# Optimization experiments

Hardware: AMD Instinct MI355X
Metric: run time of the kernel (lower is better)

Reference implementation:

```python
import jax, jax.numpy as jnp
import numpy as np

INPUT_DIM = 2
COUNT_BINS = 16
BOUND = 5.0
FLOW_LENGTH = 4
HIDDEN = 256
MULT = 4 * COUNT_BINS - 1  # 63 param groups per dim (w:K, h:K, d:K-1, lam:K)
MIN_BIN = 1e-3
MIN_DERIV = 1e-3
MIN_LAMBDA = 0.025
N = 131072


def _masks():
    input_idx = np.arange(1, INPUT_DIM + 1)                  # [2]
    hidden_idx = np.arange(HIDDEN) % (INPUT_DIM - 1) + 1     # all ones for input_dim=2
    out_idx = np.tile(input_idx, MULT)                       # [126] -> [1,2,1,2,...]
    m1 = (hidden_idx[:, None] >= input_idx[None, :]).astype(np.float32)   # [H,2]
    m2 = (hidden_idx[:, None] >= hidden_idx[None, :]).astype(np.float32)  # [H,H]
    m3 = (out_idx[:, None] > hidden_idx[None, :]).astype(np.float32)      # [126,H]
    return jnp.asarray(m1), jnp.asarray(m2), jnp.asarray(m3)


def _made(z, W1, b1, W2, b2, W3, b3, m1, m2, m3):
    # masked MLP producing raw spline params, shape [..., MULT, input_dim]
    h = jax.nn.relu(z @ (W1 * m1).T + b1)
    h = jax.nn.relu(h @ (W2 * m2).T + b2)
    out = (h @ (W3 * m3).T + b3).reshape(z.shape[:-1] + (MULT, INPUT_DIM))
    K = COUNT_BINS
    sw = lambda t: jnp.swapaxes(t, -1, -2)  # -> [..., input_dim, K]
    w = sw(out[..., 0:K, :])
    hh = sw(out[..., K:2 * K, :])
    d = sw(out[..., 2 * K:3 * K - 1, :])
    lam = sw(out[..., 3 * K - 1:4 * K - 1, :])
    return w, hh, d, lam


def _spline(x, w_raw, h_raw, d_raw, l_raw):
    # Pyro monotonic linear rational spline (Dolatabadi et al.), forward only.
    K = COUNT_BINS
    left, right = -BOUND, BOUND
    w = jax.nn.softmax(w_raw, axis=-1)
    h = jax.nn.softmax(h_raw, axis=-1)
    d = jax.nn.softplus(d_raw)
    l = jax.nn.sigmoid(l_raw)

    widths = MIN_BIN + (1.0 - MIN_BIN * K) * w
    zpad = jnp.zeros(widths.shape[:-1] + (1,), widths.dtype)
    cw = jnp.concatenate([zpad, jnp.cumsum(widths, -1)], -1)
    cw = (right - left) * cw + left
    cw = cw.at[..., 0].set(left).at[..., -1].set(right)
    widths = cw[..., 1:] - cw[..., :-1]

    heights = MIN_BIN + (1.0 - MIN_BIN * K) * h
    ch = jnp.concatenate([zpad, jnp.cumsum(heights, -1)], -1)
    ch = (right - left) * ch + left
    ch = ch.at[..., 0].set(left).at[..., -1].set(right)
    heights = ch[..., 1:] - ch[..., :-1]

    deriv = MIN_DERIV + d
    onep = jnp.ones(deriv.shape[:-1] + (1,), deriv.dtype)
    deriv = jnp.concatenate([onep, deriv, onep], -1)  # boundary derivs = 1, [.., K+1]

    lam = MIN_LAMBDA + (1.0 - 2.0 * MIN_LAMBDA) * l

    inside = (x >= left) & (x <= right)
    xc = jnp.clip(x, left, right)

    bin_idx = jnp.clip(jnp.sum((xc[..., None] >= cw).astype(jnp.int32), -1) - 1, 0, K - 1)
    ib = bin_idx[..., None]
    g = lambda t: jnp.take_along_axis(t, ib, -1)[..., 0]
    x_k = g(cw)
    w_k = g(widths)
    y_k = g(ch)
    h_k = g(heights)
    d_k = g(deriv)
    d_k1 = jnp.take_along_axis(deriv, ib + 1, -1)[..., 0]
    lam_k = g(lam)

    wa = 1.0
    wb = jnp.sqrt(d_k / d_k1) * wa
    wc = (lam_k * wa * d_k + (1.0 - lam_k) * wb * d_k1) * (w_k / h_k)
    ya = y_k
    yb = h_k + y_k
    yc = ((1.0 - lam_k) * wa * ya + lam_k * wb * yb) / ((1.0 - lam_k) * wa + lam_k * wb)

    theta = (xc - x_k) / w_k
    left_seg = theta <= lam_k
    num = jnp.where(left_seg,
                    wa * ya * (lam_k - theta) + wc * yc * theta,
                    wc * yc * (1.0 - theta) + wb * yb * (theta - lam_k))
    den = jnp.where(left_seg,
                    wa * (lam_k - theta) + wc * theta,
                    wc * (1.0 - theta) + wb * (theta - lam_k))
    y = num / den
    return jnp.where(inside, y, x)  # identity outside [-B, B]


def setup_inputs() -> dict:
    key = jax.random.key(0)
    ks = jax.random.split(key, 7)
    s = 0.05
    return {
        "x": jax.random.normal(ks[0], (N, INPUT_DIM), jnp.float32),
        "W1": jax.random.normal(ks[1], (HIDDEN, INPUT_DIM), jnp.float32) * s,
        "b1": jax.random.normal(ks[2], (HIDDEN,), jnp.float32) * s,
        "W2": jax.random.normal(ks[3], (HIDDEN, HIDDEN), jnp.float32) * s,
        "b2": jax.random.normal(ks[4], (HIDDEN,), jnp.float32) * s,
        "W3": jax.random.normal(ks[5], (MULT * INPUT_DIM, HIDDEN), jnp.float32) * s,
        "b3": jax.random.normal(ks[6], (MULT * INPUT_DIM,), jnp.float32) * s,
    }


def reference(x, W1, b1, W2, b2, W3, b3):
    # forward(): apply the SAME shared spline transform flow_length times,
    # collecting intermediates zs (returned stacked: [L+1, N, 2]).
    m1, m2, m3 = _masks()
    z = x
    zs = [z]
    for _ in range(FLOW_LENGTH):
        w, hh, d, l = _made(z, W1, b1, W2, b2, W3, b3, m1, m2, m3)
        z = _spline(z, w, hh, d, l)
        zs.append(z)
    return jnp.stack(zs)
```

## Files before the change

kernel.cpp:

```cpp
#include <hip/hip_runtime.h>
#include <math.h>

#define N_SAMPLES 131072
#define HIDDEN    256
#define M_GRID    2048
#define REC       160
#define U_LO      (-8.0f)
#define DELTA     0.0078125f
#define INV_DELTA 128.0f
#define MT3       16

__device__ float g_H2T[M_GRID * HIDDEN];
__device__ float g_table[M_GRID * REC];
__device__ float g_knots0[REC];

__device__ __forceinline__ float rcpf(float x) { return __builtin_amdgcn_rcpf(x); }

__device__ __forceinline__ float softplusf(float x) {
  return fmaxf(x, 0.0f) + log1pf(expf(-fabsf(x)));
}

__device__ void process_column(const float* __restrict__ raw, int stride,
                               float* __restrict__ rec) {
  float v[16];
  float cw[17], ch[17], dv[17], lm[16];
  float mx = -1e30f;
#pragma unroll
  for (int k = 0; k < 16; k++) { v[k] = raw[k * stride]; mx = fmaxf(mx, v[k]); }
  float s = 0.0f;
#pragma unroll
  for (int k = 0; k < 16; k++) { v[k] = expf(v[k] - mx); s += v[k]; }
  float scl = 0.984f / s;
  cw[0] = -5.0f;
  float a = 0.0f;
#pragma unroll
  for (int k = 0; k < 16; k++) {
    a += fmaf(v[k], scl, 0.001f);
    cw[k + 1] = fmaf(a, 10.0f, -5.0f);
  }
  cw[16] = 5.0f;
  mx = -1e30f;
#pragma unroll
  for (int k = 0; k < 16; k++) { v[k] = raw[(16 + k) * stride]; mx = fmaxf(mx, v[k]); }
  s = 0.0f;
#pragma unroll
  for (int k = 0; k < 16; k++) { v[k] = expf(v[k] - mx); s += v[k]; }
  scl = 0.984f / s;
  ch[0] = -5.0f;
  a = 0.0f;
#pragma unroll
  for (int k = 0; k < 16; k++) {
    a += fmaf(v[k], scl, 0.001f);
    ch[k + 1] = fmaf(a, 10.0f, -5.0f);
  }
  ch[16] = 5.0f;
  dv[0] = 1.0f; dv[16] = 1.0f;
#pragma unroll
  for (int j = 0; j < 15; j++) dv[j + 1] = 0.001f + softplusf(raw[(32 + j) * stride]);
#pragma unroll
  for (int k = 0; k < 16; k++) {
    float xx = raw[(47 + k) * stride];
    lm[k] = fmaf(0.95f, 1.0f / (1.0f + expf(-xx)), 0.025f);
  }
  float4* r4 = (float4*)rec;
  r4[0] = make_float4(cw[0], cw[1], cw[2], cw[3]);
  r4[1] = make_float4(cw[4], cw[5], cw[6], cw[7]);
  r4[2] = make_float4(cw[8], cw[9], cw[10], cw[11]);
  r4[3] = make_float4(cw[12], cw[13], cw[14], cw[15]);
  r4[4] = make_float4(cw[16], 0.0f, 0.0f, 0.0f);
#pragma unroll
  for (int k = 0; k < 16; k++) {
    r4[5 + 2 * k] = make_float4(ch[k], ch[k + 1], dv[k], dv[k + 1]);
    r4[6 + 2 * k] = make_float4(lm[k], 0.0f, 0.0f, 0.0f);
  }
}

__device__ __forceinline__ float spline_eval(float z, float xk, float xk1,
                                             float yk, float yk1,
                                             float dk, float dk1, float lam) {
  float xc = fminf(fmaxf(z, -5.0f), 5.0f);
  float wk = xk1 - xk;
  float hk = yk1 - yk;
  float wb = __builtin_amdgcn_sqrtf(dk * rcpf(dk1));
  float wc = fmaf(lam, dk, (1.0f - lam) * wb * dk1) * wk * rcpf(hk);
  float ya = yk;
  float yb = yk + hk;
  float yc = fmaf(lam * wb, yb, (1.0f - lam) * ya) * rcpf(fmaf(lam, wb, 1.0f - lam));
  float th = (xc - xk) * rcpf(wk);
  bool left = th <= lam;
  float num = left ? fmaf(ya, lam - th, wc * yc * th)
                   : fmaf(wc * yc, 1.0f - th, wb * yb * (th - lam));
  float den = left ? fmaf(wc, th, lam - th)
                   : fmaf(wc, 1.0f - th, wb * (th - lam));
  float y = num * rcpf(den);
  bool inside = (z >= -5.0f) && (z <= 5.0f);
  return inside ? y : z;
}

__global__ __launch_bounds__(256) void k_gemm2(const float* __restrict__ W1,
                                               const float* __restrict__ b1,
                                               const float* __restrict__ W2,
                                               const float* __restrict__ b2) {
  __shared__ float sW[256 * 67];
  __shared__ float sH[256 * 36];
  const int t = threadIdx.x;
  const int m0 = blockIdx.x * 32;
  const int o0 = blockIdx.y * 64;
  {
    const int ol = t >> 2, seg = t & 3;
    const float* src = W2 + (size_t)(o0 + ol) * 256 + 16 * seg;
#pragma unroll
    for (int c = 0; c < 4; c++) {
#pragma unroll
      for (int q = 0; q < 4; q++) {
        float4 v = *(const float4*)(src + 64 * c + 4 * q);
        const int k = 64 * c + 16 * seg + 4 * q;
        sW[(k + 0) * 67 + ol] = v.x;
        sW[(k + 1) * 67 + ol] = v.y;
        sW[(k + 2) * 67 + ol] = v.z;
        sW[(k + 3) * 67 + ol] = v.w;
      }
    }
  }
  {
    const float w1v = W1[2 * t];
    const float b1v = b1[t];
#pragma unroll
    for (int q = 0; q < 8; q++) {
      float4 h;
      float u0 = fmaf((float)(m0 + 4 * q + 0), DELTA, U_LO);
      float u1 = fmaf((float)(m0 + 4 * q + 1), DELTA, U_LO);
      float u2 = fmaf((float)(m0 + 4 * q + 2), DELTA, U_LO);
      float u3 = fmaf((float)(m0 + 4 * q + 3), DELTA, U_LO);
      h.x = fmaxf(fmaf(u0, w1v, b1v), 0.0f);
      h.y = fmaxf(fmaf(u1, w1v, b1v), 0.0f);
      h.z = fmaxf(fmaf(u2, w1v, b1v), 0.0f);
      h.w = fmaxf(fmaf(u3, w1v, b1v), 0.0f);
      *(float4*)&sH[t * 36 + 4 * q] = h;
    }
  }
  __syncthreads();
  const int w = t >> 6, lane = t & 63;
  const int tp = lane >> 2, tm = lane & 3;
  float acc[4][8] = {};
  const int kb = w * 64;
#pragma unroll 8
  for (int kk = 0; kk < 64; kk++) {
    const int k = kb + kk;
    float4 av = *(const float4*)&sW[k * 67 + 4 * tp];
    float4 b0 = *(const float4*)&sH[k * 36 + 8 * tm];
    float4 b1v = *(const float4*)&sH[k * 36 + 8 * tm + 4];
#pragma unroll
    for (int i = 0; i < 4; i++) {
      const float a = (i == 0) ? av.x : (i == 1) ? av.y : (i == 2) ? av.z : av.w;
      acc[i][0] = fmaf(a, b0.x, acc[i][0]);
      acc[i][1] = fmaf(a, b0.y, acc[i][1]);
      acc[i][2] = fmaf(a, b0.z, acc[i][2]);
      acc[i][3] = fmaf(a, b0.w, acc[i][3]);
      acc[i][4] = fmaf(a, b1v.x, acc[i][4]);
      acc[i][5] = fmaf(a, b1v.y, acc[i][5]);
      acc[i][6] = fmaf(a, b1v.z, acc[i][6]);
      acc[i][7] = fmaf(a, b1v.w, acc[i][7]);
    }
  }
  __syncthreads();
  if (w > 0) {
#pragma unroll
    for (int i = 0; i < 4; i++) {
      *(float4*)&sH[((w - 1) * 64 + lane) * 36 + 8 * i] =
          make_float4(acc[i][0], acc[i][1], acc[i][2], acc[i][3]);
      *(float4*)&sH[((w - 1) * 64 + lane) * 36 + 8 * i + 4] =
          make_float4(acc[i][4], acc[i][5], acc[i][6], acc[i][7]);
    }
  }
  __syncthreads();
  if (w == 0) {
#pragma unroll
    for (int v = 0; v < 3; v++) {
#pragma unroll
      for (int i = 0; i < 4; i++) {
        float4 r0 = *(const float4*)&sH[(v * 64 + lane) * 36 + 8 * i];
        float4 r1 = *(const float4*)&sH[(v * 64 + lane) * 36 + 8 * i + 4];
        acc[i][0] += r0.x; acc[i][1] += r0.y; acc[i][2] += r0.z; acc[i][3] += r0.w;
        acc[i][4] += r1.x; acc[i][5] += r1.y; acc[i][6] += r1.z; acc[i][7] += r1.w;
      }
    }
    float4 bb = *(const float4*)&b2[o0 + 4 * tp];
#pragma unroll
    for (int j = 0; j < 8; j++) {
      float4 r;
      r.x = fmaxf(acc[0][j] + bb.x, 0.0f);
      r.y = fmaxf(acc[1][j] + bb.y, 0.0f);
      r.z = fmaxf(acc[2][j] + bb.z, 0.0f);
      r.w = fmaxf(acc[3][j] + bb.w, 0.0f);
      *(float4*)&g_H2T[(size_t)(m0 + 8 * tm + j) * 256 + o0 + 4 * tp] = r;
    }
  }
}

__global__ __launch_bounds__(256) void k_gemm3proc(const float* __restrict__ W3,
                                                   const float* __restrict__ b3) {
  __shared__ float sW[256 * 67];
  __shared__ float sH[256 * 20];
  __shared__ float raws[64 * 20];
  const int t = threadIdx.x;
  const int m0 = blockIdx.x * MT3;
  {
    const int ol = t >> 2, seg = t & 3;
    const int row = (ol < 63) ? (2 * ol + 1) : 1;
    const float* src = W3 + (size_t)row * 256 + 16 * seg;
#pragma unroll
    for (int c = 0; c < 4; c++) {
#pragma unroll
      for (int q = 0; q < 4; q++) {
        float4 v = *(const float4*)(src + 64 * c + 4 * q);
        const int k = 64 * c + 16 * seg + 4 * q;
        sW[(k + 0) * 67 + ol] = v.x;
        sW[(k + 1) * 67 + ol] = v.y;
        sW[(k + 2) * 67 + ol] = v.z;
        sW[(k + 3) * 67 + ol] = v.w;
      }
    }
  }
  {
    const int j = t & 15, c = t >> 4;
    const float* src = g_H2T + (size_t)(m0 + j) * 256 + 16 * c;
#pragma unroll
    for (int q = 0; q < 4; q++) {
      float4 v = *(const float4*)(src + 4 * q);
      const int k = 16 * c + 4 * q;
      sH[(k + 0) * 20 + j] = v.x;
      sH[(k + 1) * 20 + j] = v.y;
      sH[(k + 2) * 20 + j] = v.z;
      sH[(k + 3) * 20 + j] = v.w;
    }
  }
  __syncthreads();
  const int w = t >> 6, lane = t & 63;
  const int tp = lane >> 2, tm = lane & 3;
  float acc[4][4] = {};
  const int kb = w * 64;
#pragma unroll 8
  for (int kk = 0; kk < 64; kk++) {
    const int k = kb + kk;
    float4 av = *(const float4*)&sW[k * 67 + 4 * tp];
    float4 bv = *(const float4*)&sH[k * 20 + 4 * tm];
    acc[0][0] = fmaf(av.x, bv.x, acc[0][0]); acc[0][1] = fmaf(av.x, bv.y, acc[0][1]);
    acc[0][2] = fmaf(av.x, bv.z, acc[0][2]); acc[0][3] = fmaf(av.x, bv.w, acc[0][3]);
    acc[1][0] = fmaf(av.y, bv.x, acc[1][0]); acc[1][1] = fmaf(av.y, bv.y, acc[1][1]);
    acc[1][2] = fmaf(av.y, bv.z, acc[1][2]); acc[1][3] = fmaf(av.y, bv.w, acc[1][3]);
    acc[2][0] = fmaf(av.z, bv.x, acc[2][0]); acc[2][1] = fmaf(av.z, bv.y, acc[2][1]);
    acc[2][2] = fmaf(av.z, bv.z, acc[2][2]); acc[2][3] = fmaf(av.z, bv.w, acc[2][3]);
    acc[3][0] = fmaf(av.w, bv.x, acc[3][0]); acc[3][1] = fmaf(av.w, bv.y, acc[3][1]);
    acc[3][2] = fmaf(av.w, bv.z, acc[3][2]); acc[3][3] = fmaf(av.w, bv.w, acc[3][3]);
  }
  __syncthreads();
  if (w > 0) {
#pragma unroll
    for (int i = 0; i < 4; i++)
      *(float4*)&sH[((w - 1) * 64 + lane) * 20 + 4 * i] =
          make_float4(acc[i][0], acc[i][1], acc[i][2], acc[i][3]);
  }
  __syncthreads();
  if (w == 0) {
#pragma unroll
    for (int v = 0; v < 3; v++) {
#pragma unroll
      for (int i = 0; i < 4; i++) {
        float4 r = *(const float4*)&sH[(v * 64 + lane) * 20 + 4 * i];
        acc[i][0] += r.x; acc[i][1] += r.y; acc[i][2] += r.z; acc[i][3] += r.w;
      }
    }
#pragma unroll
    for (int i = 0; i < 4; i++) {
      const int p = 4 * tp + i;
      const int bi = (p < 63) ? (2 * p + 1) : 1;
      const float bias = b3[bi];
      *(float4*)&raws[p * 20 + 4 * tm] =
          make_float4(acc[i][0] + bias, acc[i][1] + bias,
                      acc[i][2] + bias, acc[i][3] + bias);
    }
  }
  __syncthreads();
  if (t < MT3) process_column(&raws[t], 20, g_table + (size_t)(m0 + t) * REC);
  if (t == 64 && blockIdx.x == 0) process_column(b3, 2, g_knots0);
}

__global__ __launch_bounds__(256) void k_main(const float* __restrict__ x,
                                              float* __restrict__ out) {
  __shared__ float kn0[REC];
  for (int j = threadIdx.x; j < REC; j += 256) kn0[j] = g_knots0[j];
  __syncthreads();
  const int i = blockIdx.x * 256 + threadIdx.x;
  const float2 xv = ((const float2*)x)[i];
  float z0 = xv.x, z1 = xv.y;
  ((float2*)out)[i] = xv;
  for (int t = 0; t < 4; t++) {
    float tt = (z0 - U_LO) * INV_DELTA;
    int i0 = (int)floorf(tt);
    i0 = min(max(i0, 0), M_GRID - 2);
    float f = fminf(fmaxf(tt - (float)i0, 0.0f), 1.0f);
    const float* r0 = g_table + (size_t)i0 * REC;
    const float* r1 = r0 + REC;
    float cwv[17];
#pragma unroll
    for (int q = 0; q < 4; q++) {
      float4 a = *(const float4*)(r0 + 4 * q);
      float4 b = *(const float4*)(r1 + 4 * q);
      cwv[4 * q + 0] = fmaf(f, b.x - a.x, a.x);
      cwv[4 * q + 1] = fmaf(f, b.y - a.y, a.y);
      cwv[4 * q + 2] = fmaf(f, b.z - a.z, a.z);
      cwv[4 * q + 3] = fmaf(f, b.w - a.w, a.w);
    }
    cwv[16] = 5.0f;
    float xc1 = fminf(fmaxf(z1, -5.0f), 5.0f);
    int k1 = -1;
    float xk = cwv[0], xk1 = cwv[16];
    bool seen = false;
#pragma unroll
    for (int j = 0; j < 16; j++) {
      bool c = xc1 >= cwv[j];
      k1 += c ? 1 : 0;
      xk = c ? cwv[j] : xk;
      bool ff = (!c) && (!seen);
      xk1 = ff ? cwv[j] : xk1;
      seen = seen || (!c);
    }
    const float* s0 = r0 + 20 + 8 * k1;
    const float* s1 = s0 + REC;
    float4 pa = *(const float4*)s0;
    float4 pb = *(const float4*)s1;
    float la = s0[4], lb = s1[4];
    float yk  = fmaf(f, pb.x - pa.x, pa.x);
    float yk1 = fmaf(f, pb.y - pa.y, pa.y);
    float dk  = fmaf(f, pb.z - pa.z, pa.z);
    float dk1 = fmaf(f, pb.w - pa.w, pa.w);
    float lam = fmaf(f, lb - la, la);
    float z1n = spline_eval(z1, xk, xk1, yk, yk1, dk, dk1, lam);
    float xc0 = fminf(fmaxf(z0, -5.0f), 5.0f);
    int k0 = -1;
    float xk0 = kn0[0], xk01 = kn0[16];
    bool seen0 = false;
#pragma unroll
    for (int j = 0; j < 16; j++) {
      float cj = kn0[j];
      bool c = xc0 >= cj;
      k0 += c ? 1 : 0;
      xk0 = c ? cj : xk0;
      bool ff = (!c) && (!seen0);
      xk01 = ff ? cj : xk01;
      seen0 = seen0 || (!c);
    }
    const int sb = 20 + 8 * k0;
    float z0n = spline_eval(z0, xk0, xk01, kn0[sb], kn0[sb + 1],
                            kn0[sb + 2], kn0[sb + 3], kn0[sb + 4]);
    z0 = z0n; z1 = z1n;
    ((float2*)(out + (size_t)(t + 1) * (N_SAMPLES * 2)))[i] = make_float2(z0, z1);
  }
}

extern "C" void kernel_launch(void* const* d_in, const int* in_sizes, int n_in,
                              void* d_out, int out_size, void* d_ws, size_t ws_size,
                              hipStream_t stream) {
  const float* x  = (const float*)d_in[0];
  const float* W1 = (const float*)d_in[1];
  const float* b1 = (const float*)d_in[2];
  const float* W2 = (const float*)d_in[3];
  const float* b2 = (const float*)d_in[4];
  const float* W3 = (const float*)d_in[5];
  const float* b3 = (const float*)d_in[6];
  float* out = (float*)d_out;
  hipLaunchKernelGGL(k_gemm2, dim3(M_GRID / 32, 4), dim3(256), 0, stream, W1, b1, W2, b2);
  hipLaunchKernelGGL(k_gemm3proc, dim3(M_GRID / MT3), dim3(256), 0, stream, W3, b3);
  hipLaunchKernelGGL(k_main, dim3(N_SAMPLES / 256), dim3(256), 0, stream, x, out);
}
```

Baseline: 105.7 us.

## Pack spline knots as fp16 search keys and inline layer-1 activations in GEMM2

The lookup table record shrinks: bin edges used only for searching are stored as packed fp16. The exact fp32 edges move into each bin's record, so a lookup reads one row's search keys plus two adjacent rows' bin records instead of interpolating all 16 edges from both rows. The bin search becomes a simple count against fp16 keys, and layer-1 activations in the GEMM2 kernel are computed on the fly rather than staged in shared memory. This cuts memory traffic and ALU work in the main kernel, but the fp16 keys come from a single grid row without interpolation. Samples near a bin edge may therefore pick a different bin than the reference would.

After: 104.1 us. No clear change (-1.5%).

```diff
diff --git a/kernel.cpp b/kernel.cpp
--- a/kernel.cpp
+++ b/kernel.cpp
@@ -1,23 +1,32 @@
 #include <hip/hip_runtime.h>
+#include <hip/hip_fp16.h>
 #include <math.h>
 
 #define N_SAMPLES 131072
 #define HIDDEN    256
 #define M_GRID    2048
-#define REC       160
+#define REC       144
 #define U_LO      (-8.0f)
 #define DELTA     0.0078125f
 #define INV_DELTA 128.0f
 #define MT3       16
 
-__device__ float g_H2T[M_GRID * HIDDEN];
-__device__ float g_table[M_GRID * REC];
-__device__ float g_knots0[REC];
+__device__ __attribute__((aligned(16))) float g_H2T[M_GRID * HIDDEN];
+__device__ __attribute__((aligned(16))) float g_table[M_GRID * REC];
+__device__ __attribute__((aligned(16))) float g_knots0[REC];
 
 __device__ __forceinline__ float rcpf(float x) { return __builtin_amdgcn_rcpf(x); }
 
 __device__ __forceinline__ float softplusf(float x) {
   return fmaxf(x, 0.0f) + log1pf(expf(-fabsf(x)));
+}
+
+__device__ __forceinline__ void unpack8(uint4 u, float* f) {
+  float2 t;
+  t = __half22float2(*(__half2*)&u.x); f[0] = t.x; f[1] = t.y;
+  t = __half22float2(*(__half2*)&u.y); f[2] = t.x; f[3] = t.y;
+  t = __half22float2(*(__half2*)&u.z); f[4] = t.x; f[5] = t.y;
+  t = __half22float2(*(__half2*)&u.w); f[6] = t.x; f[7] = t.y;
 }
 
 __device__ void process_column(const float* __restrict__ raw, int stride,
@@ -62,16 +71,22 @@
     float xx = raw[(47 + k) * stride];
     lm[k] = fmaf(0.95f, 1.0f / (1.0f + expf(-xx)), 0.025f);
   }
+  unsigned int kn[8];
+#pragma unroll
+  for (int q = 0; q < 8; q++) {
+    __half2 h2 = __floats2half2_rn(cw[2 * q], cw[2 * q + 1]);
+    kn[q] = *(unsigned int*)&h2;
+  }
+  uint4* u4 = (uint4*)rec;
+  u4[0] = make_uint4(kn[0], kn[1], kn[2], kn[3]);
+  u4[1] = make_uint4(kn[4], kn[5], kn[6], kn[7]);
   float4* r4 = (float4*)rec;
-  r4[0] = make_float4(cw[0], cw[1], cw[2], cw[3]);
-  r4[1] = make_float4(cw[4], cw[5], cw[6], cw[7]);
-  r4[2] = make_float4(cw[8], cw[9], cw[10], cw[11]);
-  r4[3] = make_float4(cw[12], cw[13], cw[14], cw[15]);
-  r4[4] = make_float4(cw[16], 0.0f, 0.0f, 0.0f);
+  r4[2] = make_float4(0.0f, 0.0f, 0.0f, 0.0f);
+  r4[3] = make_float4(0.0f, 0.0f, 0.0f, 0.0f);
 #pragma unroll
   for (int k = 0; k < 16; k++) {
-    r4[5 + 2 * k] = make_float4(ch[k], ch[k + 1], dv[k], dv[k + 1]);
-    r4[6 + 2 * k] = make_float4(lm[k], 0.0f, 0.0f, 0.0f);
+    r4[4 + 2 * k]     = make_float4(ch[k], ch[k + 1], dv[k], dv[k + 1]);
+    r4[4 + 2 * k + 1] = make_float4(lm[k], cw[k], cw[k + 1], 0.0f);
   }
 }
 
@@ -102,7 +117,8 @@
                                                const float* __restrict__ W2,
                                                const float* __restrict__ b2) {
   __shared__ float sW[256 * 67];
-  __shared__ float sH[256 * 36];
+  __shared__ float2 sAB[256];
+  __shared__ float red[3 * 64 * 36];
   const int t = threadIdx.x;
   const int m0 = blockIdx.x * 32;
   const int o0 = blockIdx.y * 64;
@@ -122,54 +138,36 @@
       }
     }
   }
-  {
-    const float w1v = W1[2 * t];
-    const float b1v = b1[t];
-#pragma unroll
-    for (int q = 0; q < 8; q++) {
-      float4 h;
-      float u0 = fmaf((float)(m0 + 4 * q + 0), DELTA, U_LO);
-      float u1 = fmaf((float)(m0 + 4 * q + 1), DELTA, U_LO);
-      float u2 = fmaf((float)(m0 + 4 * q + 2), DELTA, U_LO);
-      float u3 = fmaf((float)(m0 + 4 * q + 3), DELTA, U_LO);
-      h.x = fmaxf(fmaf(u0, w1v, b1v), 0.0f);
-      h.y = fmaxf(fmaf(u1, w1v, b1v), 0.0f);
-      h.z = fmaxf(fmaf(u2, w1v, b1v), 0.0f);
-      h.w = fmaxf(fmaf(u3, w1v, b1v), 0.0f);
-      *(float4*)&sH[t * 36 + 4 * q] = h;
-    }
-  }
+  sAB[t] = make_float2(W1[2 * t], b1[t]);
   __syncthreads();
   const int w = t >> 6, lane = t & 63;
   const int tp = lane >> 2, tm = lane & 3;
+  const float u0 = fmaf((float)(m0 + 8 * tm), DELTA, U_LO);
   float acc[4][8] = {};
   const int kb = w * 64;
 #pragma unroll 8
   for (int kk = 0; kk < 64; kk++) {
     const int k = kb + kk;
     float4 av = *(const float4*)&sW[k * 67 + 4 * tp];
-    float4 b0 = *(const float4*)&sH[k * 36 + 8 * tm];
-    float4 b1v = *(const float4*)&sH[k * 36 + 8 * tm + 4];
+    float2 ab = sAB[k];
+    float t0 = fmaf(ab.x, u0, ab.y);
+    float st = ab.x * DELTA;
+    float h[8];
+#pragma unroll
+    for (int j = 0; j < 8; j++) h[j] = fmaxf(fmaf((float)j, st, t0), 0.0f);
 #pragma unroll
     for (int i = 0; i < 4; i++) {
-      const float a = (i == 0) ? av.x : (i == 1) ? av.y : (i == 2) ? av.z : av.w;
-      acc[i][0] = fmaf(a, b0.x, acc[i][0]);
-      acc[i][1] = fmaf(a, b0.y, acc[i][1]);
-      acc[i][2] = fmaf(a, b0.z, acc[i][2]);
-      acc[i][3] = fmaf(a, b0.w, acc[i][3]);
-      acc[i][4] = fmaf(a, b1v.x, acc[i][4]);
-      acc[i][5] = fmaf(a, b1v.y, acc[i][5]);
-      acc[i][6] = fmaf(a, b1v.z, acc[i][6]);
-      acc[i][7] = fmaf(a, b1v.w, acc[i][7]);
-    }
-  }
-  __syncthreads();
+      const float aa = (i == 0) ? av.x : (i == 1) ? av.y : (i == 2) ? av.z : av.w;
+#pragma unroll
+      for (int j = 0; j < 8; j++) acc[i][j] = fmaf(aa, h[j], acc[i][j]);
+    }
+  }
   if (w > 0) {
 #pragma unroll
     for (int i = 0; i < 4; i++) {
-      *(float4*)&sH[((w - 1) * 64 + lane) * 36 + 8 * i] =
+      *(float4*)&red[((w - 1) * 64 + lane) * 36 + 8 * i] =
           make_float4(acc[i][0], acc[i][1], acc[i][2], acc[i][3]);
-      *(float4*)&sH[((w - 1) * 64 + lane) * 36 + 8 * i + 4] =
+      *(float4*)&red[((w - 1) * 64 + lane) * 36 + 8 * i + 4] =
           make_float4(acc[i][4], acc[i][5], acc[i][6], acc[i][7]);
     }
   }
@@ -179,8 +177,8 @@
     for (int v = 0; v < 3; v++) {
 #pragma unroll
       for (int i = 0; i < 4; i++) {
-        float4 r0 = *(const float4*)&sH[(v * 64 + lane) * 36 + 8 * i];
-        float4 r1 = *(const float4*)&sH[(v * 64 + lane) * 36 + 8 * i + 4];
+        float4 r0 = *(const float4*)&red[(v * 64 + lane) * 36 + 8 * i];
+        float4 r1 = *(const float4*)&red[(v * 64 + lane) * 36 + 8 * i + 4];
         acc[i][0] += r0.x; acc[i][1] += r0.y; acc[i][2] += r0.z; acc[i][3] += r0.w;
         acc[i][4] += r1.x; acc[i][5] += r1.y; acc[i][6] += r1.z; acc[i][7] += r1.w;
       }
@@ -288,9 +286,16 @@
 
 __global__ __launch_bounds__(256) void k_main(const float* __restrict__ x,
                                               float* __restrict__ out) {
-  __shared__ float kn0[REC];
+  __shared__ __attribute__((aligned(16))) float kn0[REC];
   for (int j = threadIdx.x; j < REC; j += 256) kn0[j] = g_knots0[j];
   __syncthreads();
+  float kf0[16];
+  {
+    uint4 q0 = *(const uint4*)(kn0);
+    uint4 q1 = *(const uint4*)(kn0 + 4);
+    unpack8(q0, kf0);
+    unpack8(q1, kf0 + 8);
+  }
   const int i = blockIdx.x * 256 + threadIdx.x;
   const float2 xv = ((const float2*)x)[i];
   float z0 = xv.x, z1 = xv.y;
@@ -301,59 +306,38 @@
     i0 = min(max(i0, 0), M_GRID - 2);
     float f = fminf(fmaxf(tt - (float)i0, 0.0f), 1.0f);
     const float* r0 = g_table + (size_t)i0 * REC;
-    const float* r1 = r0 + REC;
-    float cwv[17];
-#pragma unroll
-    for (int q = 0; q < 4; q++) {
-      float4 a = *(const float4*)(r0 + 4 * q);
-      float4 b = *(const float4*)(r1 + 4 * q);
-      cwv[4 * q + 0] = fmaf(f, b.x - a.x, a.x);
-      cwv[4 * q + 1] = fmaf(f, b.y - a.y, a.y);
-      cwv[4 * q + 2] = fmaf(f, b.z - a.z, a.z);
-      cwv[4 * q + 3] = fmaf(f, b.w - a.w, a.w);
-    }
-    cwv[16] = 5.0f;
+    float kf[16];
+    {
+      uint4 q0 = *(const uint4*)(r0);
+      uint4 q1 = *(const uint4*)(r0 + 4);
+      unpack8(q0, kf);
+      unpack8(q1, kf + 8);
+    }
     float xc1 = fminf(fmaxf(z1, -5.0f), 5.0f);
-    int k1 = -1;
-    float xk = cwv[0], xk1 = cwv[16];
-    bool seen = false;
-#pragma unroll
-    for (int j = 0; j < 16; j++) {
-      bool c = xc1 >= cwv[j];
-      k1 += c ? 1 : 0;
-      xk = c ? cwv[j] : xk;
-      bool ff = (!c) && (!seen);
-      xk1 = ff ? cwv[j] : xk1;
-      seen = seen || (!c);
-    }
-    const float* s0 = r0 + 20 + 8 * k1;
-    const float* s1 = s0 + REC;
-    float4 pa = *(const float4*)s0;
-    float4 pb = *(const float4*)s1;
-    float la = s0[4], lb = s1[4];
-    float yk  = fmaf(f, pb.x - pa.x, pa.x);
-    float yk1 = fmaf(f, pb.y - pa.y, pa.y);
-    float dk  = fmaf(f, pb.z - pa.z, pa.z);
-    float dk1 = fmaf(f, pb.w - pa.w, pa.w);
-    float lam = fmaf(f, lb - la, la);
+    int k1 = 0;
+#pragma unroll
+    for (int j = 1; j < 16; j++) k1 += (xc1 >= kf[j]) ? 1 : 0;
+    const float* c0 = r0 + 16 + 8 * k1;
+    float4 A0 = *(const float4*)c0;
+    float4 A1 = *(const float4*)(c0 + 4);
+    float4 B0 = *(const float4*)(c0 + REC);
+    float4 B1 = *(const float4*)(c0 + REC + 4);
+    float yk  = fmaf(f, B0.x - A0.x, A0.x);
+    float yk1 = fmaf(f, B0.y - A0.y, A0.y);
+    float dk  = fmaf(f, B0.z - A0.z, A0.z);
+    float dk1 = fmaf(f, B0.w - A0.w, A0.w);
+    float lam = fmaf(f, B1.x - A1.x, A1.x);
+    float xk  = fmaf(f, B1.y - A1.y, A1.y);
+    float xk1 = fmaf(f, B1.z - A1.z, A1.z);
     float z1n = spline_eval(z1, xk, xk1, yk, yk1, dk, dk1, lam);
     float xc0 = fminf(fmaxf(z0, -5.0f), 5.0f);
-    int k0 = -1;
-    float xk0 = kn0[0], xk01 = kn0[16];
-    bool seen0 = false;
-#pragma unroll
-    for (int j = 0; j < 16; j++) {
-      float cj = kn0[j];
-      bool c = xc0 >= cj;
-      k0 += c ? 1 : 0;
-      xk0 = c ? cj : xk0;
-      bool ff = (!c) && (!seen0);
-      xk01 = ff ? cj : xk01;
-      seen0 = seen0 || (!c);
-    }
-    const int sb = 20 + 8 * k0;
-    float z0n = spline_eval(z0, xk0, xk01, kn0[sb], kn0[sb + 1],
-                            kn0[sb + 2], kn0[sb + 3], kn0[sb + 4]);
+    int k0 = 0;
+#pragma unroll
+    for (int j = 1; j < 16; j++) k0 += (xc0 >= kf0[j]) ? 1 : 0;
+    const float* c = kn0 + 16 + 8 * k0;
+    float4 C0 = *(const float4*)c;
+    float4 C1 = *(const float4*)(c + 4);
+    float z0n = spline_eval(z0, C1.y, C1.z, C0.x, C0.y, C0.z, C0.w, C1.x);
     z0 = z0n; z1 = z1n;
     ((float2*)(out + (size_t)(t + 1) * (N_SAMPLES * 2)))[i] = make_float2(z0, z1);
   }
```
